# Optimization experiments

Hardware: AMD Instinct MI355X
Metric: run time of the kernel (lower is better)

The kernel has to match this reference:

```python
import jax, jax.numpy as jnp
import numpy as np

H = W = 128
HW = H * W
BIG = HW  # sentinel label for background (also serves as the background 'component' id, like cv2 label 0)


def _neighbor_min(L2):
    # min over 8-connected neighborhood + self (cv2 default connectivity=8)
    Lp = jnp.pad(L2, 1, constant_values=BIG)
    m = L2
    for dr in (-1, 0, 1):
        for dc in (-1, 0, 1):
            m = jnp.minimum(m, Lp[1 + dr:1 + dr + H, 1 + dc:1 + dc + W])
    return m


def _cc_labels(fg):
    """Connected-component labeling via min-label propagation + pointer jumping.
    fg: (H,W) bool. Returns (HW,) int32: each fg pixel gets the min flat index
    of its component; bg pixels get BIG."""
    idx = jnp.arange(HW, dtype=jnp.int32)
    L0 = jnp.where(fg.reshape(-1), idx, jnp.int32(BIG))

    def step(L):
        L2 = jnp.where(fg, L.reshape(H, W), jnp.int32(BIG))
        m = jnp.where(fg, _neighbor_min(L2), jnp.int32(BIG)).reshape(-1)
        # two pointer-jumps (path compression) for fast convergence
        ext = jnp.append(m, jnp.int32(BIG))
        m = ext[m]
        m = jnp.append(m, jnp.int32(BIG))[m]
        return m

    def cond(st):
        return st[1]

    def body(st):
        L, _ = st
        Ln = step(L)
        return (Ln, jnp.any(Ln != L))

    L, _ = jax.lax.while_loop(cond, body, (L0, jnp.bool_(True)))
    return L


def _mask_loss(mask):
    # mask: (H, W) float. Faithful to torch: components computed on detached mask.
    fg = jax.lax.stop_gradient(mask) > 0
    L = _cc_labels(fg)  # (HW,) labels in [0, HW]; BIG == background component
    flat = jnp.arange(HW, dtype=jnp.int32)
    rows = flat // W
    cols = flat % W
    n = HW + 1
    area = jax.ops.segment_sum(jnp.ones(HW, jnp.int32), L, num_segments=n)
    rmin = jax.ops.segment_min(rows, L, num_segments=n)
    rmax = jax.ops.segment_max(rows, L, num_segments=n)
    cmin = jax.ops.segment_min(cols, L, num_segments=n)
    cmax = jax.ops.segment_max(cols, L, num_segments=n)
    a = jnp.where(area > 0, area, -1)
    top2_vals, top2_idx = jax.lax.top_k(a, 2)
    have2 = top2_vals[1] > 0  # len(stats) > 1 in the original
    j = top2_idx[1]           # second-largest-area component (stats[-2])
    r0, r1, c0, c1 = rmin[j], rmax[j], cmin[j], cmax[j]
    rr = jnp.arange(H)[:, None]
    cc = jnp.arange(W)[None, :]
    inbox = (rr >= r0) & (rr <= r1) & (cc >= c0) & (cc <= c1) & have2
    pmask = jnp.where(inbox, jnp.zeros((), mask.dtype), jnp.ones((), mask.dtype))
    return (pmask * mask).mean()


def setup_inputs() -> dict:
    key = jax.random.key(0)
    masks = jax.random.normal(key, (8, 16, H, W), dtype=jnp.float32)
    return {"masks": masks}


def reference(masks):
    b, k, h, w = masks.shape
    flat = masks.reshape(b * k, h, w)
    losses = jax.vmap(_mask_loss)(flat)
    return losses.mean()
```

## Files before the change

kernel.cpp:

```cpp
#include <hip/hip_runtime.h>
#include <hip/hip_bf16.h>
#include <stdint.h>

#define HH 128
#define WW 128
#define HWPX 16384
#define BIGL 16384
#define NT 1024
#define PPT 16

__device__ __forceinline__ int findRootH(int* L, int x) {
    int p = L[x];
    while (p != x) {
        int g = L[p];
        if (g != p) atomicMin(&L[x], g);
        x = p; p = g;
    }
    return x;
}
__device__ __forceinline__ int findRootF(int* L, int x) {
    int p = L[x];
    while (p != x) {
        int g = L[p];
        if (g != p) L[x] = g;
        x = p; p = g;
    }
    return p;
}
__device__ __forceinline__ void uni(int* L, int a, int b) {
    a = findRootH(L, a);
    b = findRootH(L, b);
    while (a != b) {
        if (a > b) { int t = a; a = b; b = t; }
        int old = atomicMin(&L[b], a);
        if (old == b) break;
        b = findRootH(L, old);
    }
}

__device__ __forceinline__ int wsumi(int v)    { for (int o = 32; o; o >>= 1) v += __shfl_xor(v, o, 64); return v; }
__device__ __forceinline__ float wsumf(float v){ for (int o = 32; o; o >>= 1) v += __shfl_xor(v, o, 64); return v; }
__device__ __forceinline__ int wmini(int v)    { for (int o = 32; o; o >>= 1) v = min(v, __shfl_xor(v, o, 64)); return v; }
__device__ __forceinline__ int wmaxi(int v)    { for (int o = 32; o; o >>= 1) v = max(v, __shfl_xor(v, o, 64)); return v; }

__global__ __launch_bounds__(NT)
void cc_kernel(const float* __restrict__ masks, float* __restrict__ losses) {
    __shared__ int L[HWPX];
    __shared__ unsigned rowbits[HH][4];
    __shared__ int s_bg;
    __shared__ int s_r0, s_r1, s_c0, s_c1;
    __shared__ unsigned s_k2;
    __shared__ unsigned s_wk[32];
    __shared__ float s_wsum[16];
    __shared__ float s_total;

    const int tid = threadIdx.x;
    const int lane = tid & 63;
    const int wid = tid >> 6;
    const float* msk = masks + (size_t)blockIdx.x * HWPX;
    const int base = tid * PPT;
    const int row  = base >> 7;
    const int col0 = base & 127;

    float vals[PPT];
    const float4* m4 = (const float4*)(msk + base);
#pragma unroll
    for (int q = 0; q < 4; ++q) {
        float4 v = m4[q];
        vals[q * 4 + 0] = v.x; vals[q * 4 + 1] = v.y;
        vals[q * 4 + 2] = v.z; vals[q * 4 + 3] = v.w;
    }
    unsigned fgbits = 0;
    float tsum = 0.f;
    int lab[PPT];
    {
        int start = -1;
#pragma unroll
        for (int k = 0; k < PPT; ++k) {
            tsum += vals[k];
            if (vals[k] > 0.f) {
                fgbits |= 1u << k;
                if (start < 0) start = k;
                lab[k] = base + start;
            } else {
                start = -1;
                lab[k] = BIGL;
            }
        }
    }
    {
        int4* Lv = (int4*)(L + base);
#pragma unroll
        for (int q = 0; q < 4; ++q)
            Lv[q] = make_int4(lab[q * 4], lab[q * 4 + 1], lab[q * 4 + 2], lab[q * 4 + 3]);
    }
    unsigned lf = __shfl(fgbits, lane > 0 ? lane - 1 : lane, 64);
    unsigned rf = __shfl(fgbits, lane < 63 ? lane + 1 : lane, 64);
    const unsigned leftbit  = (col0 > 0)   ? ((lf >> 15) & 1u) : 0u;
    const unsigned rightbit = (col0 < 112) ? (rf & 1u)         : 0u;
    unsigned other = __shfl_xor(fgbits, 1, 64);
    if (!(tid & 1)) rowbits[row][(tid >> 1) & 3] = fgbits | (other << 16);

    tsum = wsumf(tsum);
    if (lane == 0) s_wsum[wid] = tsum;
    if (tid == 0) { s_bg = 0; s_r0 = HH; s_r1 = -1; s_c0 = WW; s_c1 = -1; }
    __syncthreads();

    if (tid < 64) {
        float t = (tid < 16) ? s_wsum[tid] : 0.f;
        for (int o = 8; o; o >>= 1) t += __shfl_xor(t, o, 64);
        if (tid == 0) s_total = t;
    }
    if (fgbits) {
        unsigned up = 0;
        if (row > 0) {
            const int wi  = col0 >> 5;
            const int off = col0 & 31;
            unsigned w0 = rowbits[row - 1][wi];
            unsigned w1 = (wi < 3) ? rowbits[row - 1][wi + 1] : 0u;
            unsigned long long uv = ((unsigned long long)w1 << 32) | w0;
            if (off == 16) {
                up = (unsigned)(uv >> 15) & 0x3FFFFu;
            } else {
                unsigned lw = (col0 > 0) ? rowbits[row - 1][wi - 1] : 0u;
                up = (unsigned)((uv << 1) | (lw >> 31)) & 0x3FFFFu;
            }
        }
        if ((fgbits & 1u) && leftbit) uni(L, base, base - 1);
        const unsigned ULv = up & 0xFFFFu;
        const unsigned UPv = (up >> 1) & 0xFFFFu;
        const unsigned URv = (up >> 2) & 0xFFFFu;
        const unsigned lFv = ((fgbits << 1) | leftbit) & 0xFFFFu;
        const unsigned rFv = (fgbits >> 1) | (rightbit << 15);
        unsigned m = fgbits & ( (~lFv & (ULv | UPv | URv))
                              | (lFv & ((UPv & ~ULv) | (~rFv & URv & ~UPv))) );
        while (m) {
            int k = __ffs(m) - 1; m &= m - 1;
            int i = base + k;
            unsigned UL = (ULv >> k) & 1u;
            unsigned UP = (UPv >> k) & 1u;
            unsigned UR = (URv >> k) & 1u;
            unsigned lF = (lFv >> k) & 1u;
            unsigned rF = (rFv >> k) & 1u;
            if (!lF) {
                if (UL)        uni(L, i, i - WW - 1);
                if (UP && !UL) uni(L, i, i - WW);
                if (UR && !UP) uni(L, i, i - WW + 1);
            } else {
                if (UP && !UL)        uni(L, i, i - WW);
                if (!rF && UR && !UP) uni(L, i, i - WW + 1);
            }
        }
    }
    __syncthreads();

    int rr[PPT];
    int firstRoot = 0x7FFFFFFF;
    {
        int cur = -1;
#pragma unroll
        for (int k = 0; k < PPT; ++k) {
            rr[k] = -1;
            if (fgbits & (1u << k)) {
                if (k == 0 || !(fgbits & (1u << (k - 1)))) {
                    cur = findRootF(L, base + k);
                    L[base + k] = cur;
                }
                rr[k] = cur;
                if (firstRoot == 0x7FFFFFFF) firstRoot = cur;
            }
        }
    }
    __syncthreads();

    {
        const int R0 = wmini(firstRoot);
        int giant = 0, bgc = 0, prev = -1, cnt = 0;
#pragma unroll
        for (int k = 0; k < PPT; ++k) {
            if (!(fgbits & (1u << k))) { ++bgc; continue; }
            int r = rr[k];
            if (r == R0) { ++giant; }
            else if (r == prev) ++cnt;
            else {
                if (cnt) atomicAdd(&L[prev], cnt << 16);
                prev = r; cnt = 1;
            }
        }
        if (cnt) atomicAdd(&L[prev], cnt << 16);
        int g = wsumi(giant);
        if (lane == 0 && R0 != 0x7FFFFFFF && g) atomicAdd(&L[R0], g << 16);
        int b = wsumi(bgc);
        if (lane == 0 && b) atomicAdd(&s_bg, b);
    }
    __syncthreads();

    int bg = s_bg;
    unsigned b1 = 0, b2 = 0;
    if (tid == 0 && bg > 0) b1 = ((unsigned)bg << 15);
    {
        unsigned m = fgbits & ~(fgbits << 1);
        while (m) {
            int k = __ffs(m) - 1; m &= m - 1;
            int h = base + k;
            int e = L[h];
            if ((e & 0xFFFF) == h && (e >> 16) != 0) {
                unsigned key = ((unsigned)(e >> 16) << 15) | (unsigned)(BIGL - h);
                if (key > b1) { b2 = b1; b1 = key; }
                else if (key > b2) b2 = key;
            }
        }
    }
    for (int o = 32; o; o >>= 1) {
        unsigned p1 = __shfl_xor(b1, o, 64);
        unsigned p2 = __shfl_xor(b2, o, 64);
        if (p1 > b1) { b2 = (b1 > p2 ? b1 : p2); b1 = p1; }
        else if (p1 > b2) b2 = p1;
    }
    if (lane == 0) { s_wk[wid * 2] = b1; s_wk[wid * 2 + 1] = b2; }
    __syncthreads();
    if (tid < 64) {
        unsigned o1 = (tid < 16) ? s_wk[tid * 2] : 0u;
        unsigned o2 = (tid < 16) ? s_wk[tid * 2 + 1] : 0u;
        for (int o = 8; o; o >>= 1) {
            unsigned p1 = __shfl_xor(o1, o, 64);
            unsigned p2 = __shfl_xor(o2, o, 64);
            if (p1 > o1) { o2 = (o1 > p2 ? o1 : p2); o1 = p1; }
            else if (p1 > o2) o2 = p1;
        }
        if (tid == 0) s_k2 = o2;
    }
    __syncthreads();

    unsigned k2 = s_k2;
    bool have2 = (k2 >> 15) != 0;
    int j = BIGL - (int)(k2 & 0x7FFFu);

    if (have2) {
        int lc0 = WW, lc1 = -1;
#pragma unroll
        for (int k = 0; k < PPT; ++k) {
            bool inc = (fgbits & (1u << k)) ? (rr[k] == j) : (j == BIGL);
            if (inc) {
                int c = col0 + k;
                lc0 = min(lc0, c); lc1 = max(lc1, c);
            }
        }
        int lr0 = (lc1 >= 0) ? row : HH;
        int lr1 = (lc1 >= 0) ? row : -1;
        lr0 = wmini(lr0); lr1 = wmaxi(lr1);
        lc0 = wmini(lc0); lc1 = wmaxi(lc1);
        if (lane == 0 && lr1 >= 0) {
            atomicMin(&s_r0, lr0); atomicMax(&s_r1, lr1);
            atomicMin(&s_c0, lc0); atomicMax(&s_c1, lc1);
        }
    }
    __syncthreads();

    float bsum = 0.f;
    if (have2) {
        int r0 = s_r0, r1 = s_r1, c0 = s_c0, c1 = s_c1;
        if (row >= r0 && row <= r1) {
#pragma unroll
            for (int k = 0; k < PPT; ++k) {
                int c = col0 + k;
                if (c >= c0 && c <= c1) bsum += vals[k];
            }
        }
    }
    bsum = wsumf(bsum);
    __syncthreads();
    if (lane == 0) s_wsum[wid] = bsum;
    __syncthreads();
    if (tid < 64) {
        float t = (tid < 16) ? s_wsum[tid] : 0.f;
        for (int o = 8; o; o >>= 1) t += __shfl_xor(t, o, 64);
        if (tid == 0) losses[blockIdx.x] = (s_total - t) * (1.0f / 16384.0f);
    }
}

__global__ void reduce_kernel(const float* __restrict__ losses, float* __restrict__ out, int n) {
    __shared__ float s[4];
    int t = threadIdx.x;
    float v = 0.f;
    for (int i = t; i < n; i += 256) v += losses[i];
    for (int off = 32; off; off >>= 1) v += __shfl_down(v, off, 64);
    if ((t & 63) == 0) s[t >> 6] = v;
    __syncthreads();
    if (t == 0) out[0] = (s[0] + s[1] + s[2] + s[3]) / (float)n;
}

extern "C" void kernel_launch(void* const* d_in, const int* in_sizes, int n_in,
                              void* d_out, int out_size, void* d_ws, size_t ws_size,
                              hipStream_t stream) {
    const float* masks = (const float*)d_in[0];
    float* out = (float*)d_out;
    float* losses = (float*)d_ws;
    int nmask = in_sizes[0] / HWPX;
    cc_kernel<<<nmask, NT, 0, stream>>>(masks, losses);
    reduce_kernel<<<1, 256, 0, stream>>>(losses, out, nmask);
}
```

Before: 48.08 us.

## Split CC labeling into half-image blocks, then merge seam in stats kernel

The single per-mask kernel becomes two stages. The first does union-find labeling on each half image in its own block (twice the blocks, 8 pixels per thread) and writes 16-bit root labels and partial sums to workspace. The second reloads the labels, merges only across the row-64 seam, and computes component stats and the box-masked sum. The aim is more parallelism across CUs, since there are only 128 masks, and cheaper union-find per block. The cost is an extra launch plus a global round trip of the labels, and the old single-kernel path is kept as a fallback when the workspace is too small.

```diff
diff --git a/kernel.cpp b/kernel.cpp
--- a/kernel.cpp
+++ b/kernel.cpp
@@ -7,7 +7,6 @@
 #define HWPX 16384
 #define BIGL 16384
 #define NT 1024
-#define PPT 16
 
 __device__ __forceinline__ int findRootH(int* L, int x) {
     int p = L[x];
@@ -44,7 +43,129 @@
 __device__ __forceinline__ int wmaxi(int v)    { for (int o = 32; o; o >>= 1) v = max(v, __shfl_xor(v, o, 64)); return v; }
 
 __global__ __launch_bounds__(NT)
-void cc_kernel(const float* __restrict__ masks, float* __restrict__ losses) {
+void cc_half_kernel(const float* __restrict__ masks, unsigned short* __restrict__ labs,
+                    float* __restrict__ sums) {
+    __shared__ int L[8192];
+    __shared__ unsigned rowbits[64][4];
+    __shared__ float s_wsum[16];
+
+    const int tid  = threadIdx.x;
+    const int lane = tid & 63;
+    const int wid  = tid >> 6;
+    const int im   = blockIdx.x >> 1;
+    const int h    = blockIdx.x & 1;
+    const float* msk = masks + ((size_t)im << 14) + h * 8192;
+    const int base = tid * 8;
+    const int rl   = tid >> 4;
+    const int col0 = (tid & 15) * 8;
+
+    float4 v0 = ((const float4*)(msk + base))[0];
+    float4 v1 = ((const float4*)(msk + base))[1];
+    float vals[8] = {v0.x, v0.y, v0.z, v0.w, v1.x, v1.y, v1.z, v1.w};
+    unsigned fg = 0;
+    float tsum = 0.f;
+    int lab[8];
+    {
+        int start = -1;
+#pragma unroll
+        for (int k = 0; k < 8; ++k) {
+            tsum += vals[k];
+            if (vals[k] > 0.f) {
+                fg |= 1u << k;
+                if (start < 0) start = k;
+                lab[k] = base + start;
+            } else { start = -1; lab[k] = 8192; }
+        }
+    }
+    {
+        int4* Lv = (int4*)(L + base);
+        Lv[0] = make_int4(lab[0], lab[1], lab[2], lab[3]);
+        Lv[1] = make_int4(lab[4], lab[5], lab[6], lab[7]);
+    }
+    unsigned lf = __shfl(fg, lane > 0 ? lane - 1 : lane, 64);
+    unsigned rf = __shfl(fg, lane < 63 ? lane + 1 : lane, 64);
+    const unsigned leftbit  = (col0 > 0)   ? ((lf >> 7) & 1u) : 0u;
+    const unsigned rightbit = (col0 < 120) ? (rf & 1u)        : 0u;
+    unsigned b1_ = __shfl(fg, lane + 1, 64);
+    unsigned b2_ = __shfl(fg, lane + 2, 64);
+    unsigned b3_ = __shfl(fg, lane + 3, 64);
+    if ((lane & 3) == 0)
+        rowbits[rl][(tid & 15) >> 2] = fg | (b1_ << 8) | (b2_ << 16) | (b3_ << 24);
+
+    tsum = wsumf(tsum);
+    if (lane == 0) s_wsum[wid] = tsum;
+    __syncthreads();
+    if (tid < 64) {
+        float t = (tid < 16) ? s_wsum[tid] : 0.f;
+        for (int o = 8; o; o >>= 1) t += __shfl_xor(t, o, 64);
+        if (tid == 0) sums[im * 2 + h] = t;
+    }
+
+    if (fg) {
+        unsigned up10 = 0;
+        if (rl > 0) {
+            const int wi  = col0 >> 5;
+            const int off = col0 & 31;
+            unsigned w0 = rowbits[rl - 1][wi];
+            unsigned w1 = (wi < 3) ? rowbits[rl - 1][wi + 1] : 0u;
+            unsigned long long uv = ((unsigned long long)w1 << 32) | w0;
+            if (off) up10 = (unsigned)(uv >> (off - 1)) & 0x3FFu;
+            else {
+                unsigned lw = wi ? rowbits[rl - 1][wi - 1] : 0u;
+                up10 = (unsigned)((uv << 1) | (lw >> 31)) & 0x3FFu;
+            }
+        }
+        if ((fg & 1u) && leftbit) uni(L, base, base - 1);
+        const unsigned ULv = up10 & 0xFFu;
+        const unsigned UPv = (up10 >> 1) & 0xFFu;
+        const unsigned URv = (up10 >> 2) & 0xFFu;
+        const unsigned lFv = ((fg << 1) | leftbit) & 0xFFu;
+        const unsigned rFv = (fg >> 1) | (rightbit << 7);
+        unsigned m = fg & ( (~lFv & (ULv | UPv | URv))
+                          | (lFv & ((UPv & ~ULv) | (~rFv & URv & ~UPv))) );
+        while (m) {
+            int k = __ffs(m) - 1; m &= m - 1;
+            int i = base + k;
+            unsigned UL = (ULv >> k) & 1u;
+            unsigned UP = (UPv >> k) & 1u;
+            unsigned UR = (URv >> k) & 1u;
+            unsigned lF = (lFv >> k) & 1u;
+            unsigned rF = (rFv >> k) & 1u;
+            if (!lF) {
+                if (UL)        uni(L, i, i - WW - 1);
+                if (UP && !UL) uni(L, i, i - WW);
+                if (UR && !UP) uni(L, i, i - WW + 1);
+            } else {
+                if (UP && !UL)        uni(L, i, i - WW);
+                if (!rF && UR && !UP) uni(L, i, i - WW + 1);
+            }
+        }
+    }
+    __syncthreads();
+
+    const int off16 = h * 8192;
+    unsigned short o[8];
+    {
+        int cur = -1;
+#pragma unroll
+        for (int k = 0; k < 8; ++k) {
+            if (fg & (1u << k)) {
+                if (k == 0 || !(fg & (1u << (k - 1)))) cur = findRootF(L, base + k);
+                o[k] = (unsigned short)(cur + off16);
+            } else o[k] = 0xFFFFu;
+        }
+    }
+    int4 w;
+    w.x = (int)o[0] | ((int)o[1] << 16);
+    w.y = (int)o[2] | ((int)o[3] << 16);
+    w.z = (int)o[4] | ((int)o[5] << 16);
+    w.w = (int)o[6] | ((int)o[7] << 16);
+    ((int4*)(labs + ((size_t)im << 14) + off16 + base))[0] = w;
+}
+
+__global__ __launch_bounds__(NT)
+void cc_stats_kernel(const float* __restrict__ masks, const unsigned short* __restrict__ labs,
+                     const float* __restrict__ sums, float* __restrict__ losses) {
     __shared__ int L[HWPX];
     __shared__ unsigned rowbits[HH][4];
     __shared__ int s_bg;
@@ -54,45 +175,33 @@
     __shared__ float s_wsum[16];
     __shared__ float s_total;
 
-    const int tid = threadIdx.x;
+    const int tid  = threadIdx.x;
     const int lane = tid & 63;
-    const int wid = tid >> 6;
-    const float* msk = masks + (size_t)blockIdx.x * HWPX;
-    const int base = tid * PPT;
+    const int wid  = tid >> 6;
+    const int im   = blockIdx.x;
+    const int base = tid * 16;
     const int row  = base >> 7;
     const int col0 = base & 127;
 
-    float vals[PPT];
-    const float4* m4 = (const float4*)(msk + base);
-#pragma unroll
-    for (int q = 0; q < 4; ++q) {
-        float4 v = m4[q];
-        vals[q * 4 + 0] = v.x; vals[q * 4 + 1] = v.y;
-        vals[q * 4 + 2] = v.z; vals[q * 4 + 3] = v.w;
-    }
+    const int4* lp = (const int4*)(labs + ((size_t)im << 14) + base);
+    int4 a = lp[0], b = lp[1];
+    int li[16];
+    li[0]=a.x&0xFFFF; li[1]=(a.x>>16)&0xFFFF; li[2]=a.y&0xFFFF; li[3]=(a.y>>16)&0xFFFF;
+    li[4]=a.z&0xFFFF; li[5]=(a.z>>16)&0xFFFF; li[6]=a.w&0xFFFF; li[7]=(a.w>>16)&0xFFFF;
+    li[8]=b.x&0xFFFF; li[9]=(b.x>>16)&0xFFFF; li[10]=b.y&0xFFFF; li[11]=(b.y>>16)&0xFFFF;
+    li[12]=b.z&0xFFFF; li[13]=(b.z>>16)&0xFFFF; li[14]=b.w&0xFFFF; li[15]=(b.w>>16)&0xFFFF;
     unsigned fgbits = 0;
-    float tsum = 0.f;
-    int lab[PPT];
-    {
-        int start = -1;
-#pragma unroll
-        for (int k = 0; k < PPT; ++k) {
-            tsum += vals[k];
-            if (vals[k] > 0.f) {
-                fgbits |= 1u << k;
-                if (start < 0) start = k;
-                lab[k] = base + start;
-            } else {
-                start = -1;
-                lab[k] = BIGL;
-            }
-        }
+    int lab[16];
+#pragma unroll
+    for (int k = 0; k < 16; ++k) {
+        if (li[k] != 0xFFFF) { fgbits |= 1u << k; lab[k] = li[k]; }
+        else lab[k] = BIGL;
     }
     {
         int4* Lv = (int4*)(L + base);
 #pragma unroll
         for (int q = 0; q < 4; ++q)
-            Lv[q] = make_int4(lab[q * 4], lab[q * 4 + 1], lab[q * 4 + 2], lab[q * 4 + 3]);
+            Lv[q] = make_int4(lab[q*4], lab[q*4+1], lab[q*4+2], lab[q*4+3]);
     }
     unsigned lf = __shfl(fgbits, lane > 0 ? lane - 1 : lane, 64);
     unsigned rf = __shfl(fgbits, lane < 63 ? lane + 1 : lane, 64);
@@ -100,12 +209,243 @@
     const unsigned rightbit = (col0 < 112) ? (rf & 1u)         : 0u;
     unsigned other = __shfl_xor(fgbits, 1, 64);
     if (!(tid & 1)) rowbits[row][(tid >> 1) & 3] = fgbits | (other << 16);
+    if (tid == 0) {
+        s_bg = 0; s_r0 = HH; s_r1 = -1; s_c0 = WW; s_c1 = -1;
+        s_total = sums[im * 2] + sums[im * 2 + 1];
+    }
+    __syncthreads();
+
+    if (row == 64 && fgbits) {
+        unsigned up = 0;
+        {
+            const int wi  = col0 >> 5;
+            const int off = col0 & 31;
+            unsigned w0 = rowbits[63][wi];
+            unsigned w1 = (wi < 3) ? rowbits[63][wi + 1] : 0u;
+            unsigned long long uv = ((unsigned long long)w1 << 32) | w0;
+            if (off == 16) up = (unsigned)(uv >> 15) & 0x3FFFFu;
+            else {
+                unsigned lw = (col0 > 0) ? rowbits[63][wi - 1] : 0u;
+                up = (unsigned)((uv << 1) | (lw >> 31)) & 0x3FFFFu;
+            }
+        }
+        const unsigned ULv = up & 0xFFFFu;
+        const unsigned UPv = (up >> 1) & 0xFFFFu;
+        const unsigned URv = (up >> 2) & 0xFFFFu;
+        const unsigned lFv = ((fgbits << 1) | leftbit) & 0xFFFFu;
+        const unsigned rFv = (fgbits >> 1) | (rightbit << 15);
+        unsigned m = fgbits & ( (~lFv & (ULv | UPv | URv))
+                              | (lFv & ((UPv & ~ULv) | (~rFv & URv & ~UPv))) );
+        while (m) {
+            int k = __ffs(m) - 1; m &= m - 1;
+            int i = base + k;
+            unsigned UL = (ULv >> k) & 1u;
+            unsigned UP = (UPv >> k) & 1u;
+            unsigned UR = (URv >> k) & 1u;
+            unsigned lF = (lFv >> k) & 1u;
+            unsigned rF = (rFv >> k) & 1u;
+            if (!lF) {
+                if (UL)        uni(L, i, i - WW - 1);
+                if (UP && !UL) uni(L, i, i - WW);
+                if (UR && !UP) uni(L, i, i - WW + 1);
+            } else {
+                if (UP && !UL)        uni(L, i, i - WW);
+                if (!rF && UR && !UP) uni(L, i, i - WW + 1);
+            }
+        }
+    }
+    __syncthreads();
+
+    int rr[16];
+    int firstRoot = 0x7FFFFFFF;
+    {
+        int cur = -1;
+#pragma unroll
+        for (int k = 0; k < 16; ++k) {
+            rr[k] = -1;
+            if (fgbits & (1u << k)) {
+                if (k == 0 || !(fgbits & (1u << (k - 1)))) {
+                    cur = findRootF(L, base + k);
+                    L[base + k] = cur;
+                }
+                rr[k] = cur;
+                if (firstRoot == 0x7FFFFFFF) firstRoot = cur;
+            }
+        }
+    }
+    __syncthreads();
+
+    {
+        const int R0 = wmini(firstRoot);
+        int giant = 0, bgc = 0, prev = -1, cnt = 0;
+#pragma unroll
+        for (int k = 0; k < 16; ++k) {
+            if (!(fgbits & (1u << k))) { ++bgc; continue; }
+            int r = rr[k];
+            if (r == R0) ++giant;
+            else if (r == prev) ++cnt;
+            else {
+                if (cnt) atomicAdd(&L[prev], cnt << 16);
+                prev = r; cnt = 1;
+            }
+        }
+        if (cnt) atomicAdd(&L[prev], cnt << 16);
+        int g = wsumi(giant);
+        if (lane == 0 && R0 != 0x7FFFFFFF && g) atomicAdd(&L[R0], g << 16);
+        int bq = wsumi(bgc);
+        if (lane == 0 && bq) atomicAdd(&s_bg, bq);
+    }
+    __syncthreads();
+
+    int bg = s_bg;
+    unsigned b1 = 0, b2 = 0;
+    if (tid == 0 && bg > 0) b1 = ((unsigned)bg << 15);
+    {
+        unsigned m = fgbits & ~(fgbits << 1);
+        while (m) {
+            int k = __ffs(m) - 1; m &= m - 1;
+            int hh = base + k;
+            int e = L[hh];
+            if ((e & 0xFFFF) == hh && (e >> 16) != 0) {
+                unsigned key = ((unsigned)(e >> 16) << 15) | (unsigned)(BIGL - hh);
+                if (key > b1) { b2 = b1; b1 = key; }
+                else if (key > b2) b2 = key;
+            }
+        }
+    }
+    for (int o = 32; o; o >>= 1) {
+        unsigned p1 = __shfl_xor(b1, o, 64);
+        unsigned p2 = __shfl_xor(b2, o, 64);
+        if (p1 > b1) { b2 = (b1 > p2 ? b1 : p2); b1 = p1; }
+        else if (p1 > b2) b2 = p1;
+    }
+    if (lane == 0) { s_wk[wid * 2] = b1; s_wk[wid * 2 + 1] = b2; }
+    __syncthreads();
+    if (tid < 64) {
+        unsigned o1 = (tid < 16) ? s_wk[tid * 2] : 0u;
+        unsigned o2 = (tid < 16) ? s_wk[tid * 2 + 1] : 0u;
+        for (int o = 8; o; o >>= 1) {
+            unsigned p1 = __shfl_xor(o1, o, 64);
+            unsigned p2 = __shfl_xor(o2, o, 64);
+            if (p1 > o1) { o2 = (o1 > p2 ? o1 : p2); o1 = p1; }
+            else if (p1 > o2) o2 = p1;
+        }
+        if (tid == 0) s_k2 = o2;
+    }
+    __syncthreads();
+
+    unsigned k2 = s_k2;
+    bool have2 = (k2 >> 15) != 0;
+    int j = BIGL - (int)(k2 & 0x7FFFu);
+
+    if (have2) {
+        int lc0 = WW, lc1 = -1;
+#pragma unroll
+        for (int k = 0; k < 16; ++k) {
+            bool inc = (fgbits & (1u << k)) ? (rr[k] == j) : (j == BIGL);
+            if (inc) {
+                int c = col0 + k;
+                lc0 = min(lc0, c); lc1 = max(lc1, c);
+            }
+        }
+        int lr0 = (lc1 >= 0) ? row : HH;
+        int lr1 = (lc1 >= 0) ? row : -1;
+        lr0 = wmini(lr0); lr1 = wmaxi(lr1);
+        lc0 = wmini(lc0); lc1 = wmaxi(lc1);
+        if (lane == 0 && lr1 >= 0) {
+            atomicMin(&s_r0, lr0); atomicMax(&s_r1, lr1);
+            atomicMin(&s_c0, lc0); atomicMax(&s_c1, lc1);
+        }
+    }
+    __syncthreads();
+
+    float bsum = 0.f;
+    if (have2) {
+        int r0 = s_r0, r1 = s_r1, c0 = s_c0, c1 = s_c1;
+        if (row >= r0 && row <= r1) {
+            const float* msk = masks + ((size_t)im << 14);
+            const float4* m4 = (const float4*)(msk + base);
+#pragma unroll
+            for (int q = 0; q < 4; ++q) {
+                float4 v = m4[q];
+                float vv[4] = {v.x, v.y, v.z, v.w};
+#pragma unroll
+                for (int t = 0; t < 4; ++t) {
+                    int c = col0 + q * 4 + t;
+                    if (c >= c0 && c <= c1) bsum += vv[t];
+                }
+            }
+        }
+    }
+    bsum = wsumf(bsum);
+    __syncthreads();
+    if (lane == 0) s_wsum[wid] = bsum;
+    __syncthreads();
+    if (tid < 64) {
+        float t = (tid < 16) ? s_wsum[tid] : 0.f;
+        for (int o = 8; o; o >>= 1) t += __shfl_xor(t, o, 64);
+        if (tid == 0) losses[im] = (s_total - t) * (1.0f / 16384.0f);
+    }
+}
+
+__global__ __launch_bounds__(NT)
+void cc_fallback(const float* __restrict__ masks, float* __restrict__ losses) {
+    __shared__ int L[HWPX];
+    __shared__ unsigned rowbits[HH][4];
+    __shared__ int s_bg;
+    __shared__ int s_r0, s_r1, s_c0, s_c1;
+    __shared__ unsigned s_k2;
+    __shared__ unsigned s_wk[32];
+    __shared__ float s_wsum[16];
+    __shared__ float s_total;
+
+    const int tid = threadIdx.x;
+    const int lane = tid & 63;
+    const int wid = tid >> 6;
+    const float* msk = masks + (size_t)blockIdx.x * HWPX;
+    const int base = tid * 16;
+    const int row  = base >> 7;
+    const int col0 = base & 127;
+
+    float vals[16];
+    const float4* m4 = (const float4*)(msk + base);
+#pragma unroll
+    for (int q = 0; q < 4; ++q) {
+        float4 v = m4[q];
+        vals[q*4+0]=v.x; vals[q*4+1]=v.y; vals[q*4+2]=v.z; vals[q*4+3]=v.w;
+    }
+    unsigned fgbits = 0;
+    float tsum = 0.f;
+    int lab[16];
+    {
+        int start = -1;
+#pragma unroll
+        for (int k = 0; k < 16; ++k) {
+            tsum += vals[k];
+            if (vals[k] > 0.f) {
+                fgbits |= 1u << k;
+                if (start < 0) start = k;
+                lab[k] = base + start;
+            } else { start = -1; lab[k] = BIGL; }
+        }
+    }
+    {
+        int4* Lv = (int4*)(L + base);
+#pragma unroll
+        for (int q = 0; q < 4; ++q)
+            Lv[q] = make_int4(lab[q*4], lab[q*4+1], lab[q*4+2], lab[q*4+3]);
+    }
+    unsigned lf = __shfl(fgbits, lane > 0 ? lane - 1 : lane, 64);
+    unsigned rf = __shfl(fgbits, lane < 63 ? lane + 1 : lane, 64);
+    const unsigned leftbit  = (col0 > 0)   ? ((lf >> 15) & 1u) : 0u;
+    const unsigned rightbit = (col0 < 112) ? (rf & 1u)         : 0u;
+    unsigned other = __shfl_xor(fgbits, 1, 64);
+    if (!(tid & 1)) rowbits[row][(tid >> 1) & 3] = fgbits | (other << 16);
 
     tsum = wsumf(tsum);
     if (lane == 0) s_wsum[wid] = tsum;
     if (tid == 0) { s_bg = 0; s_r0 = HH; s_r1 = -1; s_c0 = WW; s_c1 = -1; }
     __syncthreads();
-
     if (tid < 64) {
         float t = (tid < 16) ? s_wsum[tid] : 0.f;
         for (int o = 8; o; o >>= 1) t += __shfl_xor(t, o, 64);
@@ -119,9 +459,8 @@
             unsigned w0 = rowbits[row - 1][wi];
             unsigned w1 = (wi < 3) ? rowbits[row - 1][wi + 1] : 0u;
             unsigned long long uv = ((unsigned long long)w1 << 32) | w0;
-            if (off == 16) {
-                up = (unsigned)(uv >> 15) & 0x3FFFFu;
-            } else {
+            if (off == 16) up = (unsigned)(uv >> 15) & 0x3FFFFu;
+            else {
                 unsigned lw = (col0 > 0) ? rowbits[row - 1][wi - 1] : 0u;
                 up = (unsigned)((uv << 1) | (lw >> 31)) & 0x3FFFFu;
             }
@@ -153,13 +492,12 @@
         }
     }
     __syncthreads();
-
-    int rr[PPT];
+    int rr[16];
     int firstRoot = 0x7FFFFFFF;
     {
         int cur = -1;
 #pragma unroll
-        for (int k = 0; k < PPT; ++k) {
+        for (int k = 0; k < 16; ++k) {
             rr[k] = -1;
             if (fgbits & (1u << k)) {
                 if (k == 0 || !(fgbits & (1u << (k - 1)))) {
@@ -172,15 +510,14 @@
         }
     }
     __syncthreads();
-
     {
         const int R0 = wmini(firstRoot);
         int giant = 0, bgc = 0, prev = -1, cnt = 0;
 #pragma unroll
-        for (int k = 0; k < PPT; ++k) {
+        for (int k = 0; k < 16; ++k) {
             if (!(fgbits & (1u << k))) { ++bgc; continue; }
             int r = rr[k];
-            if (r == R0) { ++giant; }
+            if (r == R0) ++giant;
             else if (r == prev) ++cnt;
             else {
                 if (cnt) atomicAdd(&L[prev], cnt << 16);
@@ -190,11 +527,10 @@
         if (cnt) atomicAdd(&L[prev], cnt << 16);
         int g = wsumi(giant);
         if (lane == 0 && R0 != 0x7FFFFFFF && g) atomicAdd(&L[R0], g << 16);
-        int b = wsumi(bgc);
-        if (lane == 0 && b) atomicAdd(&s_bg, b);
-    }
-    __syncthreads();
-
+        int bq = wsumi(bgc);
+        if (lane == 0 && bq) atomicAdd(&s_bg, bq);
+    }
+    __syncthreads();
     int bg = s_bg;
     unsigned b1 = 0, b2 = 0;
     if (tid == 0 && bg > 0) b1 = ((unsigned)bg << 15);
@@ -202,10 +538,10 @@
         unsigned m = fgbits & ~(fgbits << 1);
         while (m) {
             int k = __ffs(m) - 1; m &= m - 1;
-            int h = base + k;
-            int e = L[h];
-            if ((e & 0xFFFF) == h && (e >> 16) != 0) {
-                unsigned key = ((unsigned)(e >> 16) << 15) | (unsigned)(BIGL - h);
+            int hh = base + k;
+            int e = L[hh];
+            if ((e & 0xFFFF) == hh && (e >> 16) != 0) {
+                unsigned key = ((unsigned)(e >> 16) << 15) | (unsigned)(BIGL - hh);
                 if (key > b1) { b2 = b1; b1 = key; }
                 else if (key > b2) b2 = key;
             }
@@ -231,15 +567,13 @@
         if (tid == 0) s_k2 = o2;
     }
     __syncthreads();
-
     unsigned k2 = s_k2;
     bool have2 = (k2 >> 15) != 0;
     int j = BIGL - (int)(k2 & 0x7FFFu);
-
     if (have2) {
         int lc0 = WW, lc1 = -1;
 #pragma unroll
-        for (int k = 0; k < PPT; ++k) {
+        for (int k = 0; k < 16; ++k) {
             bool inc = (fgbits & (1u << k)) ? (rr[k] == j) : (j == BIGL);
             if (inc) {
                 int c = col0 + k;
@@ -256,13 +590,12 @@
         }
     }
     __syncthreads();
-
     float bsum = 0.f;
     if (have2) {
         int r0 = s_r0, r1 = s_r1, c0 = s_c0, c1 = s_c1;
         if (row >= r0 && row <= r1) {
 #pragma unroll
-            for (int k = 0; k < PPT; ++k) {
+            for (int k = 0; k < 16; ++k) {
                 int c = col0 + k;
                 if (c >= c0 && c <= c1) bsum += vals[k];
             }
@@ -295,8 +628,21 @@
                               hipStream_t stream) {
     const float* masks = (const float*)d_in[0];
     float* out = (float*)d_out;
-    float* losses = (float*)d_ws;
     int nmask = in_sizes[0] / HWPX;
-    cc_kernel<<<nmask, NT, 0, stream>>>(masks, losses);
-    reduce_kernel<<<1, 256, 0, stream>>>(losses, out, nmask);
-}
+    char* w = (char*)d_ws;
+    size_t labBytes  = (size_t)nmask * HWPX * 2;
+    size_t sumsBytes = (size_t)nmask * 2 * 4;
+    size_t need = labBytes + sumsBytes + (size_t)nmask * 4;
+    if (ws_size >= need) {
+        unsigned short* labs = (unsigned short*)w;
+        float* sums   = (float*)(w + labBytes);
+        float* losses = (float*)(w + labBytes + sumsBytes);
+        cc_half_kernel<<<nmask * 2, NT, 0, stream>>>(masks, labs, sums);
+        cc_stats_kernel<<<nmask, NT, 0, stream>>>(masks, labs, sums, losses);
+        reduce_kernel<<<1, 256, 0, stream>>>(losses, out, nmask);
+    } else {
+        float* losses = (float*)d_ws;
+        cc_fallback<<<nmask, NT, 0, stream>>>(masks, losses);
+        reduce_kernel<<<1, 256, 0, stream>>>(losses, out, nmask);
+    }
+}
```

Result: slower. 51.54 us (+7.2%).

## Split connected-component labeling into per-strip blocks plus a merge kernel

Applied to the files above, without the earlier changes.

Labeling moves from one block per 128x128 mask to eight blocks per mask, each labeling a 16-row strip in shared memory. Each strip block writes compact 16-bit labels and per-root area records to workspace. A second kernel merges the strips at their boundary rows, combines the areas, and computes the bounding box and loss. The goal is more parallelism, since there are only 128 masks for a GPU with many CUs, at the cost of an extra launch, global workspace traffic and a second read of the mask. The old single-kernel path is kept as a fallback when the workspace is too small.

```diff
diff --git a/kernel.cpp b/kernel.cpp
--- a/kernel.cpp
+++ b/kernel.cpp
@@ -7,7 +7,7 @@
 #define HWPX 16384
 #define BIGL 16384
 #define NT 1024
-#define PPT 16
+#define INFI 0x7FFFFFFF
 
 __device__ __forceinline__ int findRootH(int* L, int x) {
     int p = L[x];
@@ -22,6 +22,15 @@
     int p = L[x];
     while (p != x) {
         int g = L[p];
+        if (g != p) L[x] = g;
+        x = p; p = g;
+    }
+    return p;
+}
+__device__ __forceinline__ int findRootM(int* L, int x) {
+    int p = L[x] & 0xFFFF;
+    while (p != x) {
+        int g = L[p] & 0xFFFF;
         if (g != p) L[x] = g;
         x = p; p = g;
     }
@@ -44,7 +53,319 @@
 __device__ __forceinline__ int wmaxi(int v)    { for (int o = 32; o; o >>= 1) v = max(v, __shfl_xor(v, o, 64)); return v; }
 
 __global__ __launch_bounds__(NT)
-void cc_kernel(const float* __restrict__ masks, float* __restrict__ losses) {
+void cc_strip_kernel(const float* __restrict__ masks, unsigned* __restrict__ labs32,
+                     unsigned* __restrict__ recs, int* __restrict__ counts,
+                     float* __restrict__ sums) {
+    __shared__ int L[2048];
+    __shared__ unsigned long long rb0[16], rb1[16];
+    __shared__ float s_wsum[16];
+    __shared__ int s_cnt;
+
+    const int tid  = threadIdx.x;
+    const int lane = tid & 63;
+    const int wv   = tid >> 6;
+    const int strip = blockIdx.x;
+    const int im = strip >> 3, s = strip & 7;
+    const float* msk = masks + ((size_t)im << 14) + (s << 11);
+    const int i0 = tid * 2;
+
+    float2 v = ((const float2*)(msk + i0))[0];
+    unsigned fg = (v.x > 0.f ? 1u : 0u) | (v.y > 0.f ? 2u : 0u);
+    float tsum = v.x + v.y;
+
+    int lab1 = (fg & 2) ? ((fg & 1) ? i0 : i0 + 1) : (i0 + 1);
+    ((int2*)(L + i0))[0] = make_int2(i0, lab1);
+
+    unsigned long long b0 = __ballot(fg & 1);
+    unsigned long long b1 = __ballot(fg & 2);
+    if (lane == 0) { rb0[wv] = b0; rb1[wv] = b1; }
+    const unsigned leftbit  = (lane > 0)  ? (unsigned)((b1 >> (lane - 1)) & 1) : 0u;
+    const unsigned rightbit = (lane < 63) ? (unsigned)((b0 >> (lane + 1)) & 1) : 0u;
+
+    tsum = wsumf(tsum);
+    if (lane == 0) s_wsum[wv] = tsum;
+    if (tid == 0) s_cnt = 0;
+    __syncthreads();
+
+    if (tid < 64) {
+        float t = (tid < 16) ? s_wsum[tid] : 0.f;
+        for (int o = 8; o; o >>= 1) t += __shfl_xor(t, o, 64);
+        if (tid == 0) sums[strip] = t;
+    }
+
+    if ((fg & 1) && leftbit) uni(L, i0, i0 - 1);
+    if (fg && wv > 0) {
+        unsigned long long u0 = rb0[wv - 1], u1 = rb1[wv - 1];
+        unsigned UP0 = (unsigned)((u0 >> lane) & 1);
+        unsigned UR0 = (unsigned)((u1 >> lane) & 1);
+        unsigned UL0 = (lane > 0)  ? (unsigned)((u1 >> (lane - 1)) & 1) : 0u;
+        unsigned UR1 = (lane < 63) ? (unsigned)((u0 >> (lane + 1)) & 1) : 0u;
+        if (fg & 1) {
+            if (!leftbit) {
+                if (UL0)         uni(L, i0, i0 - 129);
+                if (UP0 && !UL0) uni(L, i0, i0 - 128);
+                if (UR0 && !UP0) uni(L, i0, i0 - 127);
+            } else {
+                if (UP0 && !UL0)              uni(L, i0, i0 - 128);
+                if (!(fg & 2) && UR0 && !UP0) uni(L, i0, i0 - 127);
+            }
+        }
+        if (fg & 2) {
+            if (!(fg & 1)) {
+                if (UP0)         uni(L, i0 + 1, i0 - 128);
+                if (UR0 && !UP0) uni(L, i0 + 1, i0 - 127);
+                if (UR1 && !UR0) uni(L, i0 + 1, i0 - 126);
+            } else {
+                if (UR0 && !UP0)              uni(L, i0 + 1, i0 - 127);
+                if (!rightbit && UR1 && !UR0) uni(L, i0 + 1, i0 - 126);
+            }
+        }
+    }
+    __syncthreads();
+
+    int rr0 = -1, rr1 = -1;
+    if (fg & 1) { rr0 = findRootF(L, i0); L[i0] = rr0; }
+    if (fg & 2) {
+        if (fg & 1) rr1 = rr0;
+        else { rr1 = findRootF(L, i0 + 1); L[i0 + 1] = rr1; }
+    }
+    int fr = (rr0 >= 0) ? rr0 : ((rr1 >= 0) ? rr1 : INFI);
+    __syncthreads();
+
+    {
+        const int R0 = wmini(fr);
+        int giant = 0;
+        if (fg == 3u) {
+            if (rr0 == R0) giant = 2; else atomicAdd(&L[rr0], 2 << 16);
+        } else {
+            if (fg & 1) { if (rr0 == R0) ++giant; else atomicAdd(&L[rr0], 1 << 16); }
+            if (fg & 2) { if (rr1 == R0) ++giant; else atomicAdd(&L[rr1], 1 << 16); }
+        }
+        int g = wsumi(giant);
+        if (lane == 0 && R0 != INFI && g) atomicAdd(&L[R0], g << 16);
+    }
+    __syncthreads();
+
+    if (fg & 1) {
+        int e = L[i0];
+        if ((e & 0xFFFF) == i0 && (e >> 16)) {
+            int x = atomicAdd(&s_cnt, 1);
+            recs[(strip << 9) + x] = ((unsigned)e & 0xFFFF0000u) | (unsigned)i0;
+        }
+    }
+    if (fg == 2u) {
+        int e = L[i0 + 1];
+        if ((e & 0xFFFF) == (i0 + 1) && (e >> 16)) {
+            int x = atomicAdd(&s_cnt, 1);
+            recs[(strip << 9) + x] = ((unsigned)e & 0xFFFF0000u) | (unsigned)(i0 + 1);
+        }
+    }
+    {
+        unsigned lo = (fg & 1) ? (unsigned)((s << 11) + rr0) : 0xFFFFu;
+        unsigned hi = (fg & 2) ? (unsigned)((s << 11) + rr1) : 0xFFFFu;
+        labs32[((size_t)im << 13) + (s << 10) + tid] = lo | (hi << 16);
+    }
+    __syncthreads();
+    if (tid == 0) counts[strip] = s_cnt;
+}
+
+__global__ __launch_bounds__(NT)
+void cc_stats2(const float* __restrict__ masks, const unsigned* __restrict__ labs32,
+               const unsigned* __restrict__ recs, const int* __restrict__ counts,
+               const float* __restrict__ sums, float* __restrict__ losses) {
+    __shared__ int L[HWPX];
+    __shared__ unsigned s_wk[32];
+    __shared__ int s_wi[16];
+    __shared__ float s_wsum[16];
+    __shared__ int s_cnt8[8];
+    __shared__ int s_r0, s_r1, s_c0, s_c1;
+    __shared__ unsigned s_k2;
+    __shared__ float s_total;
+
+    const int tid  = threadIdx.x;
+    const int lane = tid & 63;
+    const int wid  = tid >> 6;
+    const int im   = blockIdx.x;
+    const int row  = tid >> 3;
+    const int col0 = (tid & 7) * 16;
+
+    const uint4* lp = (const uint4*)(labs32 + ((size_t)im << 13));
+    uint4 A = lp[tid * 2], B = lp[tid * 2 + 1];
+    int lb[16];
+    lb[0]=A.x&0xFFFF; lb[1]=A.x>>16; lb[2]=A.y&0xFFFF; lb[3]=A.y>>16;
+    lb[4]=A.z&0xFFFF; lb[5]=A.z>>16; lb[6]=A.w&0xFFFF; lb[7]=A.w>>16;
+    lb[8]=B.x&0xFFFF; lb[9]=B.x>>16; lb[10]=B.y&0xFFFF; lb[11]=B.y>>16;
+    lb[12]=B.z&0xFFFF; lb[13]=B.z>>16; lb[14]=B.w&0xFFFF; lb[15]=B.w>>16;
+    unsigned fgbits = 0;
+#pragma unroll
+    for (int k = 0; k < 16; ++k) fgbits |= (lb[k] != 0xFFFF) ? (1u << k) : 0u;
+
+    {
+        int b16 = tid * 16;
+        int4* Lv = (int4*)(L + b16);
+#pragma unroll
+        for (int q = 0; q < 4; ++q)
+            Lv[q] = make_int4(b16 + q*4, b16 + q*4 + 1, b16 + q*4 + 2, b16 + q*4 + 3);
+    }
+    if (tid < 8) s_cnt8[tid] = counts[im * 8 + tid];
+    if (tid == 0) {
+        s_r0 = HH; s_r1 = -1; s_c0 = WW; s_c1 = -1;
+        float t = 0.f;
+        for (int q = 0; q < 8; ++q) t += sums[im * 8 + q];
+        s_total = t;
+    }
+    __syncthreads();
+
+    if (row > 0 && (row & 15) == 0 && fgbits) {
+        const unsigned short* labsu = (const unsigned short*)(labs32 + ((size_t)im << 13));
+        int up[18];
+        unsigned upb = 0;
+#pragma unroll
+        for (int d = 0; d < 18; ++d) {
+            int c = col0 + d - 1;
+            int lv = (c >= 0 && c < WW) ? (int)labsu[(row - 1) * WW + c] : 0xFFFF;
+            up[d] = lv;
+            upb |= (lv != 0xFFFF) ? (1u << d) : 0u;
+        }
+        unsigned leftb  = (col0 > 0)   ? (labsu[row * WW + col0 - 1]  != 0xFFFF) : 0u;
+        unsigned rightb = (col0 < 112) ? (labsu[row * WW + col0 + 16] != 0xFFFF) : 0u;
+        const unsigned ULv = upb & 0xFFFFu;
+        const unsigned UPv = (upb >> 1) & 0xFFFFu;
+        const unsigned URv = (upb >> 2) & 0xFFFFu;
+        const unsigned lFv = ((fgbits << 1) | leftb) & 0xFFFFu;
+        const unsigned rFv = (fgbits >> 1) | (rightb << 15);
+        unsigned m = fgbits & ( (~lFv & (ULv | UPv | URv))
+                              | (lFv & ((UPv & ~ULv) | (~rFv & URv & ~UPv))) );
+        while (m) {
+            int k = __ffs(m) - 1; m &= m - 1;
+            unsigned UL = (ULv >> k) & 1u, UP = (UPv >> k) & 1u, UR = (URv >> k) & 1u;
+            unsigned lF = (lFv >> k) & 1u, rF = (rFv >> k) & 1u;
+            if (!lF) {
+                if (UL)        uni(L, lb[k], up[k]);
+                if (UP && !UL) uni(L, lb[k], up[k + 1]);
+                if (UR && !UP) uni(L, lb[k], up[k + 2]);
+            } else {
+                if (UP && !UL)        uni(L, lb[k], up[k + 1]);
+                if (!rF && UR && !UP) uni(L, lb[k], up[k + 2]);
+            }
+        }
+    }
+    __syncthreads();
+
+    for (int s = 0; s < 8; ++s) {
+        int c = s_cnt8[s];
+        for (int i = tid; i < c; i += NT) {
+            unsigned rec = recs[((im * 8 + s) << 9) + i];
+            int lab = (s << 11) + (int)(rec & 0xFFFFu);
+            int r = findRootM(L, lab);
+            if (lab != r) L[lab] = r;
+            atomicAdd(&L[r], (int)(rec >> 16) << 16);
+        }
+    }
+    __syncthreads();
+
+    unsigned b1 = 0, b2 = 0;
+    int fgsum = 0;
+    for (int s = 0; s < 8; ++s) {
+        int c = s_cnt8[s];
+        for (int i = tid; i < c; i += NT) {
+            unsigned rec = recs[((im * 8 + s) << 9) + i];
+            int lab = (s << 11) + (int)(rec & 0xFFFFu);
+            fgsum += (int)(rec >> 16);
+            int e = L[lab];
+            if ((e & 0xFFFF) == lab && (e >> 16)) {
+                unsigned key = ((unsigned)(e >> 16) << 15) | (unsigned)(BIGL - lab);
+                if (key > b1) { b2 = b1; b1 = key; }
+                else if (key > b2) b2 = key;
+            }
+        }
+    }
+    for (int o = 32; o; o >>= 1) {
+        unsigned p1 = __shfl_xor(b1, o, 64);
+        unsigned p2 = __shfl_xor(b2, o, 64);
+        if (p1 > b1) { b2 = (b1 > p2 ? b1 : p2); b1 = p1; }
+        else if (p1 > b2) b2 = p1;
+    }
+    fgsum = wsumi(fgsum);
+    if (lane == 0) { s_wk[wid * 2] = b1; s_wk[wid * 2 + 1] = b2; s_wi[wid] = fgsum; }
+    __syncthreads();
+    if (tid < 64) {
+        unsigned o1 = (tid < 16) ? s_wk[tid * 2] : 0u;
+        unsigned o2 = (tid < 16) ? s_wk[tid * 2 + 1] : 0u;
+        int fs = (tid < 16) ? s_wi[tid] : 0;
+        for (int o = 8; o; o >>= 1) {
+            unsigned p1 = __shfl_xor(o1, o, 64);
+            unsigned p2 = __shfl_xor(o2, o, 64);
+            if (p1 > o1) { o2 = (o1 > p2 ? o1 : p2); o1 = p1; }
+            else if (p1 > o2) o2 = p1;
+            fs += __shfl_xor(fs, o, 64);
+        }
+        if (tid == 0) {
+            int bg = HWPX - fs;
+            if (bg > 0) {
+                unsigned key = (unsigned)bg << 15;
+                if (key > o1) { o2 = o1; o1 = key; }
+                else if (key > o2) o2 = key;
+            }
+            s_k2 = o2;
+        }
+    }
+    __syncthreads();
+
+    unsigned k2 = s_k2;
+    bool have2 = (k2 >> 15) != 0;
+    int j = BIGL - (int)(k2 & 0x7FFFu);
+
+    if (have2) {
+        int lc0 = WW, lc1 = -1;
+#pragma unroll
+        for (int k = 0; k < 16; ++k) {
+            bool in;
+            if (fgbits & (1u << k)) in = ((L[lb[k]] & 0xFFFF) == j);
+            else                    in = (j == BIGL);
+            if (in) { int c = col0 + k; lc0 = min(lc0, c); lc1 = max(lc1, c); }
+        }
+        int lr0 = (lc1 >= 0) ? row : HH;
+        int lr1 = (lc1 >= 0) ? row : -1;
+        lr0 = wmini(lr0); lr1 = wmaxi(lr1);
+        lc0 = wmini(lc0); lc1 = wmaxi(lc1);
+        if (lane == 0 && lr1 >= 0) {
+            atomicMin(&s_r0, lr0); atomicMax(&s_r1, lr1);
+            atomicMin(&s_c0, lc0); atomicMax(&s_c1, lc1);
+        }
+    }
+    __syncthreads();
+
+    float bsum = 0.f;
+    if (have2) {
+        int r0 = s_r0, r1 = s_r1, c0 = s_c0, c1 = s_c1;
+        if (row >= r0 && row <= r1) {
+            const float4* m4 = (const float4*)(masks + ((size_t)im << 14) + tid * 16);
+#pragma unroll
+            for (int q = 0; q < 4; ++q) {
+                float4 v = m4[q];
+                float vv[4] = {v.x, v.y, v.z, v.w};
+#pragma unroll
+                for (int t = 0; t < 4; ++t) {
+                    int c = col0 + q * 4 + t;
+                    if (c >= c0 && c <= c1) bsum += vv[t];
+                }
+            }
+        }
+    }
+    bsum = wsumf(bsum);
+    __syncthreads();
+    if (lane == 0) s_wsum[wid] = bsum;
+    __syncthreads();
+    if (tid < 64) {
+        float t = (tid < 16) ? s_wsum[tid] : 0.f;
+        for (int o = 8; o; o >>= 1) t += __shfl_xor(t, o, 64);
+        if (tid == 0) losses[im] = (s_total - t) * (1.0f / 16384.0f);
+    }
+}
+
+__global__ __launch_bounds__(NT)
+void cc_fallback(const float* __restrict__ masks, float* __restrict__ losses) {
     __shared__ int L[HWPX];
     __shared__ unsigned rowbits[HH][4];
     __shared__ int s_bg;
@@ -58,41 +379,37 @@
     const int lane = tid & 63;
     const int wid = tid >> 6;
     const float* msk = masks + (size_t)blockIdx.x * HWPX;
-    const int base = tid * PPT;
+    const int base = tid * 16;
     const int row  = base >> 7;
     const int col0 = base & 127;
 
-    float vals[PPT];
+    float vals[16];
     const float4* m4 = (const float4*)(msk + base);
 #pragma unroll
     for (int q = 0; q < 4; ++q) {
         float4 v = m4[q];
-        vals[q * 4 + 0] = v.x; vals[q * 4 + 1] = v.y;
-        vals[q * 4 + 2] = v.z; vals[q * 4 + 3] = v.w;
+        vals[q*4+0]=v.x; vals[q*4+1]=v.y; vals[q*4+2]=v.z; vals[q*4+3]=v.w;
     }
     unsigned fgbits = 0;
     float tsum = 0.f;
-    int lab[PPT];
+    int lab[16];
     {
         int start = -1;
 #pragma unroll
-        for (int k = 0; k < PPT; ++k) {
+        for (int k = 0; k < 16; ++k) {
             tsum += vals[k];
             if (vals[k] > 0.f) {
                 fgbits |= 1u << k;
                 if (start < 0) start = k;
                 lab[k] = base + start;
-            } else {
-                start = -1;
-                lab[k] = BIGL;
-            }
+            } else { start = -1; lab[k] = BIGL; }
         }
     }
     {
         int4* Lv = (int4*)(L + base);
 #pragma unroll
         for (int q = 0; q < 4; ++q)
-            Lv[q] = make_int4(lab[q * 4], lab[q * 4 + 1], lab[q * 4 + 2], lab[q * 4 + 3]);
+            Lv[q] = make_int4(lab[q*4], lab[q*4+1], lab[q*4+2], lab[q*4+3]);
     }
     unsigned lf = __shfl(fgbits, lane > 0 ? lane - 1 : lane, 64);
     unsigned rf = __shfl(fgbits, lane < 63 ? lane + 1 : lane, 64);
@@ -105,7 +422,6 @@
     if (lane == 0) s_wsum[wid] = tsum;
     if (tid == 0) { s_bg = 0; s_r0 = HH; s_r1 = -1; s_c0 = WW; s_c1 = -1; }
     __syncthreads();
-
     if (tid < 64) {
         float t = (tid < 16) ? s_wsum[tid] : 0.f;
         for (int o = 8; o; o >>= 1) t += __shfl_xor(t, o, 64);
@@ -119,9 +435,8 @@
             unsigned w0 = rowbits[row - 1][wi];
             unsigned w1 = (wi < 3) ? rowbits[row - 1][wi + 1] : 0u;
             unsigned long long uv = ((unsigned long long)w1 << 32) | w0;
-            if (off == 16) {
-                up = (unsigned)(uv >> 15) & 0x3FFFFu;
-            } else {
+            if (off == 16) up = (unsigned)(uv >> 15) & 0x3FFFFu;
+            else {
                 unsigned lw = (col0 > 0) ? rowbits[row - 1][wi - 1] : 0u;
                 up = (unsigned)((uv << 1) | (lw >> 31)) & 0x3FFFFu;
             }
@@ -153,13 +468,12 @@
         }
     }
     __syncthreads();
-
-    int rr[PPT];
-    int firstRoot = 0x7FFFFFFF;
+    int rr[16];
+    int firstRoot = INFI;
     {
         int cur = -1;
 #pragma unroll
-        for (int k = 0; k < PPT; ++k) {
+        for (int k = 0; k < 16; ++k) {
             rr[k] = -1;
             if (fgbits & (1u << k)) {
                 if (k == 0 || !(fgbits & (1u << (k - 1)))) {
@@ -167,20 +481,19 @@
                     L[base + k] = cur;
                 }
                 rr[k] = cur;
-                if (firstRoot == 0x7FFFFFFF) firstRoot = cur;
-            }
-        }
-    }
-    __syncthreads();
-
+                if (firstRoot == INFI) firstRoot = cur;
+            }
+        }
+    }
+    __syncthreads();
     {
         const int R0 = wmini(firstRoot);
         int giant = 0, bgc = 0, prev = -1, cnt = 0;
 #pragma unroll
-        for (int k = 0; k < PPT; ++k) {
+        for (int k = 0; k < 16; ++k) {
             if (!(fgbits & (1u << k))) { ++bgc; continue; }
             int r = rr[k];
-            if (r == R0) { ++giant; }
+            if (r == R0) ++giant;
             else if (r == prev) ++cnt;
             else {
                 if (cnt) atomicAdd(&L[prev], cnt << 16);
@@ -189,12 +502,11 @@
         }
         if (cnt) atomicAdd(&L[prev], cnt << 16);
         int g = wsumi(giant);
-        if (lane == 0 && R0 != 0x7FFFFFFF && g) atomicAdd(&L[R0], g << 16);
-        int b = wsumi(bgc);
-        if (lane == 0 && b) atomicAdd(&s_bg, b);
-    }
-    __syncthreads();
-
+        if (lane == 0 && R0 != INFI && g) atomicAdd(&L[R0], g << 16);
+        int bq = wsumi(bgc);
+        if (lane == 0 && bq) atomicAdd(&s_bg, bq);
+    }
+    __syncthreads();
     int bg = s_bg;
     unsigned b1 = 0, b2 = 0;
     if (tid == 0 && bg > 0) b1 = ((unsigned)bg << 15);
@@ -202,10 +514,10 @@
         unsigned m = fgbits & ~(fgbits << 1);
         while (m) {
             int k = __ffs(m) - 1; m &= m - 1;
-            int h = base + k;
-            int e = L[h];
-            if ((e & 0xFFFF) == h && (e >> 16) != 0) {
-                unsigned key = ((unsigned)(e >> 16) << 15) | (unsigned)(BIGL - h);
+            int hh = base + k;
+            int e = L[hh];
+            if ((e & 0xFFFF) == hh && (e >> 16) != 0) {
+                unsigned key = ((unsigned)(e >> 16) << 15) | (unsigned)(BIGL - hh);
                 if (key > b1) { b2 = b1; b1 = key; }
                 else if (key > b2) b2 = key;
             }
@@ -231,15 +543,13 @@
         if (tid == 0) s_k2 = o2;
     }
     __syncthreads();
-
     unsigned k2 = s_k2;
     bool have2 = (k2 >> 15) != 0;
     int j = BIGL - (int)(k2 & 0x7FFFu);
-
     if (have2) {
         int lc0 = WW, lc1 = -1;
 #pragma unroll
-        for (int k = 0; k < PPT; ++k) {
+        for (int k = 0; k < 16; ++k) {
             bool inc = (fgbits & (1u << k)) ? (rr[k] == j) : (j == BIGL);
             if (inc) {
                 int c = col0 + k;
@@ -256,13 +566,12 @@
         }
     }
     __syncthreads();
-
     float bsum = 0.f;
     if (have2) {
         int r0 = s_r0, r1 = s_r1, c0 = s_c0, c1 = s_c1;
         if (row >= r0 && row <= r1) {
 #pragma unroll
-            for (int k = 0; k < PPT; ++k) {
+            for (int k = 0; k < 16; ++k) {
                 int c = col0 + k;
                 if (c >= c0 && c <= c1) bsum += vals[k];
             }
@@ -295,8 +604,26 @@
                               hipStream_t stream) {
     const float* masks = (const float*)d_in[0];
     float* out = (float*)d_out;
-    float* losses = (float*)d_ws;
     int nmask = in_sizes[0] / HWPX;
-    cc_kernel<<<nmask, NT, 0, stream>>>(masks, losses);
-    reduce_kernel<<<1, 256, 0, stream>>>(losses, out, nmask);
-}
+    char* w = (char*)d_ws;
+    size_t labsB = (size_t)nmask * HWPX * 2;
+    size_t recsB = (size_t)nmask * 8 * 512 * 4;
+    size_t cntB  = (size_t)nmask * 8 * 4;
+    size_t sumB  = (size_t)nmask * 8 * 4;
+    size_t lossB = (size_t)nmask * 4;
+    size_t need = labsB + recsB + cntB + sumB + lossB;
+    if (ws_size >= need) {
+        unsigned* labs32 = (unsigned*)w;
+        unsigned* recs   = (unsigned*)(w + labsB);
+        int*      counts = (int*)(w + labsB + recsB);
+        float*    sums   = (float*)(w + labsB + recsB + cntB);
+        float*    losses = (float*)(w + labsB + recsB + cntB + sumB);
+        cc_strip_kernel<<<nmask * 8, NT, 0, stream>>>(masks, labs32, recs, counts, sums);
+        cc_stats2<<<nmask, NT, 0, stream>>>(masks, labs32, recs, counts, sums, losses);
+        reduce_kernel<<<1, 256, 0, stream>>>(losses, out, nmask);
+    } else {
+        float* losses = (float*)d_ws;
+        cc_fallback<<<nmask, NT, 0, stream>>>(masks, losses);
+        reduce_kernel<<<1, 256, 0, stream>>>(losses, out, nmask);
+    }
+}
```

Result: slower. 78.76 us (+63.8%).
